# Kernel tuning notes

Hardware: AMD Instinct MI355X
Metric: run time of the kernel (lower is better)

The kernel has to match this reference:

```python
import jax, jax.numpy as jnp
import numpy as np

N = 10000          # num nodes
E = 640000         # num edges (avg degree 64)
IN_CH = 128
OUT_CH = 128


def setup_inputs() -> dict:
    key = jax.random.key(0)
    k_x, k_ei, k_ea, k_w1, k_b1, k_w2, k_b2 = jax.random.split(key, 7)
    x = jax.random.normal(k_x, (N, IN_CH), dtype=jnp.float32)
    edge_index = jax.random.randint(k_ei, (2, E), 0, N, dtype=jnp.int64)
    edge_attr = jax.random.uniform(k_ea, (E,), dtype=jnp.float32)
    # MLP params: Linear(2*in, out) -> ReLU -> Linear(out, out), stored as [in, out]
    s1 = 1.0 / np.sqrt(2 * IN_CH)
    s2 = 1.0 / np.sqrt(OUT_CH)
    W1 = jax.random.uniform(k_w1, (2 * IN_CH, OUT_CH), jnp.float32, -s1, s1)
    b1 = jax.random.uniform(k_b1, (OUT_CH,), jnp.float32, -s1, s1)
    W2 = jax.random.uniform(k_w2, (OUT_CH, OUT_CH), jnp.float32, -s2, s2)
    b2 = jax.random.uniform(k_b2, (OUT_CH,), jnp.float32, -s2, s2)
    return {"x": x, "edge_index": edge_index, "edge_attr": edge_attr,
            "W1": W1, "b1": b1, "W2": W2, "b2": b2}


def reference(x, edge_index, edge_attr, W1, b1, W2, b2):
    row, col = edge_index[0], edge_index[1]
    # message: scale sender feature by edge_attr, concat with receiver feature, 2-layer MLP
    x_i = x[row] * edge_attr[:, None]          # [E, in]
    x_j = x[col]                               # [E, in]
    combined = jnp.concatenate([x_i, x_j], axis=1)  # [E, 2*in]
    h = jax.nn.relu(combined @ W1 + b1)        # [E, out]
    messages = h @ W2 + b2                     # [E, out]
    # sum aggregation: scatter-add messages into receiving nodes (col)
    out = jnp.zeros((x.shape[0], messages.shape[1]), dtype=messages.dtype)
    out = out.at[col].add(messages)
    return out
```

## Files before the change

### kernel.cpp

```cpp
#include <hip/hip_runtime.h>

#define C 128
#define NPB 16
#define NSLAB 8
#define CAP8 24
#define OVF_MAX 65536
#define EPT 4

typedef int   vi4 __attribute__((ext_vector_type(4)));
typedef float vf4 __attribute__((ext_vector_type(4)));

__device__ __forceinline__ unsigned bf16_bits(float x) {
    unsigned u = __float_as_uint(x);
    u += 0x7FFFu + ((u >> 16) & 1u);
    return u >> 16;
}
__device__ __forceinline__ float bf16f(unsigned short b) {
    return __uint_as_float(((unsigned)b) << 16);
}
__device__ __forceinline__ int xcd_id() {
    return (int)(__builtin_amdgcn_s_getreg(63508) & 7u);
}

__global__ void fused_pre_kernel(const float* __restrict__ x, const float* __restrict__ W1,
                                 unsigned short* __restrict__ P16, float* __restrict__ Q,
                                 const int* __restrict__ ei, const float* __restrict__ attr,
                                 int* __restrict__ cursor, int* __restrict__ ovf_cnt,
                                 int2* __restrict__ ovf, unsigned* __restrict__ sorted,
                                 int N, int E, int SB) {
    if ((int)blockIdx.x < SB) {
        const int slab = xcd_id();
        int* __restrict__ cur = cursor + (size_t)slab * N;
        unsigned* __restrict__ sl = sorted + ((size_t)slab * N) * CAP8;
        const int base = (blockIdx.x * 256 + threadIdx.x) * EPT;
        if (base >= E) return;
        if (base + EPT <= E) {
            const vi4 r0 = __builtin_nontemporal_load((const vi4*)(ei + base));
            const vi4 c0 = __builtin_nontemporal_load((const vi4*)(ei + (size_t)E + base));
            const vf4 a0 = __builtin_nontemporal_load((const vf4*)(attr + base));
            const int rows[EPT] = {r0.x, r0.y, r0.z, r0.w};
            const int cols[EPT] = {c0.x, c0.y, c0.z, c0.w};
            const float as[EPT] = {a0.x, a0.y, a0.z, a0.w};
            int pos[EPT];
#pragma unroll
            for (int j = 0; j < EPT; ++j)
                pos[j] = atomicAdd(&cur[cols[j]], 1);
#pragma unroll
            for (int j = 0; j < EPT; ++j) {
                const unsigned v = (bf16_bits(as[j]) << 16) | (unsigned)rows[j];
                if (pos[j] < CAP8) {
                    sl[(size_t)cols[j] * CAP8 + pos[j]] = v;
                } else {
                    const int o = atomicAdd(ovf_cnt, 1);
                    if (o < OVF_MAX) ovf[o] = make_int2(cols[j], (int)v);
                }
            }
        } else {
            for (int e = base; e < E; ++e) {
                const int row = ei[e], colv = ei[(size_t)E + e];
                const int pos = atomicAdd(&cur[colv], 1);
                const unsigned v = (bf16_bits(attr[e]) << 16) | (unsigned)row;
                if (pos < CAP8) sl[(size_t)colv * CAP8 + pos] = v;
                else {
                    const int o = atomicAdd(ovf_cnt, 1);
                    if (o < OVF_MAX) ovf[o] = make_int2(colv, (int)v);
                }
            }
        }
    } else {
        __shared__ float xs[NPB][C];
        const int pb = blockIdx.x - SB;
        const int n0 = pb * NPB;
        const int tt = threadIdx.x & (C - 1);
        const int half = threadIdx.x >> 7;
        for (int i = threadIdx.x; i < NPB * C; i += 256) {
            const int gi = n0 * C + i;
            xs[0][i] = (gi < N * C) ? __builtin_nontemporal_load(x + gi) : 0.f;
        }
        __syncthreads();
        const float* __restrict__ Wb = W1 + (half ? (C * C) : 0) + tt;
        float acc[NPB] = {};
        for (int k = 0; k < C; ++k) {
            const float w = Wb[k * C];
#pragma unroll
            for (int j = 0; j < NPB; ++j)
                acc[j] = fmaf(xs[j][k], w, acc[j]);
        }
#pragma unroll
        for (int j = 0; j < NPB; ++j)
            if (n0 + j < N) {
                if (half) Q[(size_t)(n0 + j) * C + tt] = acc[j];
                else      P16[(size_t)(n0 + j) * C + tt] = (unsigned short)bf16_bits(acc[j]);
            }
    }
}

struct G { ushort4 p; float a; };
__device__ __forceinline__ G gat(unsigned v, const unsigned short* __restrict__ P16, int ch4) {
    G g;
    g.p = *(const ushort4*)(P16 + (((size_t)(v & 0xFFFFu)) << 7) + (ch4 << 2));
    g.a = __uint_as_float(v & 0xFFFF0000u);
    return g;
}
__device__ __forceinline__ void upd(float4& acc, const G& g, const float4& qb) {
    acc.x += fmaxf(fmaf(g.a, bf16f(g.p.x), qb.x), 0.f);
    acc.y += fmaxf(fmaf(g.a, bf16f(g.p.y), qb.y), 0.f);
    acc.z += fmaxf(fmaf(g.a, bf16f(g.p.z), qb.z), 0.f);
    acc.w += fmaxf(fmaf(g.a, bf16f(g.p.w), qb.w), 0.f);
}

__global__ void agg_out_kernel(const unsigned* __restrict__ sorted, const int* __restrict__ cursor,
                               const unsigned short* __restrict__ P16, const float* __restrict__ Q,
                               const float* __restrict__ b1, const float* __restrict__ W2,
                               const float* __restrict__ b2,
                               const int* __restrict__ ovf_cnt, const int2* __restrict__ ovf,
                               float* __restrict__ out, int N) {
    __shared__ float4 part[2][4][32];
    __shared__ float hs[2][C];
    const int t = threadIdx.x;
    const int j = t >> 7;
    const int slice = (t >> 5) & 3;
    const int ch4 = t & 31;
    const int n = blockIdx.x * 2 + j;

    float4 acc = make_float4(0.f, 0.f, 0.f, 0.f);
    float4 qb = acc;
    int deg = 0;
    if (n < N) {
        int cnts[NSLAB];
#pragma unroll
        for (int s = 0; s < NSLAB; ++s) {
            cnts[s] = cursor[(size_t)s * N + n];
            deg += cnts[s];
        }
        const float4 q4  = *(const float4*)(Q + (size_t)n * C + (ch4 << 2));
        const float4 b14 = *(const float4*)(b1 + (ch4 << 2));
        qb = make_float4(q4.x + b14.x, q4.y + b14.y, q4.z + b14.z, q4.w + b14.w);
#pragma unroll
        for (int si = 0; si < 2; ++si) {
            const int s = slice + (si << 2);
            const int cs = min(cnts[s], CAP8);
            const unsigned* __restrict__ buf = sorted + ((size_t)s * N + n) * CAP8;
            int i = 0;
            for (; i + 4 <= cs; i += 4) {
                const uint4 v = *(const uint4*)(buf + i);
                const G g0 = gat(v.x, P16, ch4), g1 = gat(v.y, P16, ch4);
                const G g2 = gat(v.z, P16, ch4), g3 = gat(v.w, P16, ch4);
                upd(acc, g0, qb); upd(acc, g1, qb); upd(acc, g2, qb); upd(acc, g3, qb);
            }
            for (; i < cs; ++i) {
                const G g = gat(buf[i], P16, ch4);
                upd(acc, g, qb);
            }
        }
        const int oc = min(*ovf_cnt, OVF_MAX);
        if (oc > 0 && slice == 0) {
            for (int o = 0; o < oc; ++o) {
                const int2 v = ovf[o];
                if (v.x == n) { const G g = gat((unsigned)v.y, P16, ch4); upd(acc, g, qb); }
            }
        }
    }
    part[j][slice][ch4] = acc;
    __syncthreads();
    if (slice == 0 && n < N) {
        const float4 r0 = part[j][0][ch4], r1 = part[j][1][ch4];
        const float4 r2 = part[j][2][ch4], r3 = part[j][3][ch4];
        float4 h;
        h.x = r0.x + r1.x + r2.x + r3.x;
        h.y = r0.y + r1.y + r2.y + r3.y;
        h.z = r0.z + r1.z + r2.z + r3.z;
        h.w = r0.w + r1.w + r2.w + r3.w;
        *(float4*)(&hs[j][ch4 << 2]) = h;
    }
    __syncthreads();
    float4 o = make_float4(0.f, 0.f, 0.f, 0.f);
    if (n < N) {
        const int k0 = slice << 5;
#pragma unroll 8
        for (int k = k0; k < k0 + 32; ++k) {
            const float hv = hs[j][k];
            const float4 w = *(const float4*)(W2 + (size_t)k * C + (ch4 << 2));
            o.x = fmaf(hv, w.x, o.x);
            o.y = fmaf(hv, w.y, o.y);
            o.z = fmaf(hv, w.z, o.z);
            o.w = fmaf(hv, w.w, o.w);
        }
    }
    __syncthreads();
    part[j][slice][ch4] = o;
    __syncthreads();
    if (slice == 0 && n < N) {
        const float4 r0 = part[j][0][ch4], r1 = part[j][1][ch4];
        const float4 r2 = part[j][2][ch4], r3 = part[j][3][ch4];
        const float4 b24 = *(const float4*)(b2 + (ch4 << 2));
        const float d = (float)deg;
        float4 res;
        res.x = fmaf(d, b24.x, r0.x + r1.x + r2.x + r3.x);
        res.y = fmaf(d, b24.y, r0.y + r1.y + r2.y + r3.y);
        res.z = fmaf(d, b24.z, r0.z + r1.z + r2.z + r3.z);
        res.w = fmaf(d, b24.w, r0.w + r1.w + r2.w + r3.w);
        *(float4*)(out + (size_t)n * C + (ch4 << 2)) = res;
    }
}

extern "C" void kernel_launch(void* const* d_in, const int* in_sizes, int n_in,
                              void* d_out, int out_size, void* d_ws, size_t ws_size,
                              hipStream_t stream) {
    const float* x    = (const float*)d_in[0];
    const int*   ei   = (const int*)d_in[1];
    const float* attr = (const float*)d_in[2];
    const float* W1   = (const float*)d_in[3];
    const float* b1   = (const float*)d_in[4];
    const float* W2   = (const float*)d_in[5];
    const float* b2   = (const float*)d_in[6];
    float* out = (float*)d_out;

    const int N = in_sizes[0] / C;
    const int E = in_sizes[2];

    char* ws = (char*)d_ws;
    unsigned short* P16 = (unsigned short*)ws;  ws += (size_t)N * C * sizeof(unsigned short);
    ws = (char*)(((uintptr_t)ws + 15) & ~(uintptr_t)15);
    float*    Q       = (float*)ws;     ws += (size_t)N * C * sizeof(float);
    unsigned* sorted  = (unsigned*)ws;  ws += (size_t)NSLAB * N * CAP8 * sizeof(unsigned);
    int2*     ovf     = (int2*)ws;      ws += (size_t)OVF_MAX * sizeof(int2);
    int*      cursor  = (int*)ws;       ws += (size_t)NSLAB * N * sizeof(int);
    int*      ovf_cnt = (int*)ws;

    (void)hipMemsetAsync(cursor, 0, ((size_t)NSLAB * N + 1) * sizeof(int), stream);

    const int SB = (E + 256 * EPT - 1) / (256 * EPT);
    const int PB = (N + NPB - 1) / NPB;
    fused_pre_kernel<<<SB + PB, 256, 0, stream>>>(x, W1, P16, Q, ei, attr,
                                                  cursor, ovf_cnt, ovf, sorted, N, E, SB);
    agg_out_kernel<<<(N + 1) / 2, 256, 0, stream>>>(sorted, cursor, P16, Q, b1, W2, b2,
                                                    ovf_cnt, ovf, out, N);
}
```

Baseline: 161.3 us.

## Assign one 16-lane group per slab in aggregation and halve edges per thread in bucketing

```diff
diff --git a/kernel.cpp b/kernel.cpp
--- a/kernel.cpp
+++ b/kernel.cpp
@@ -5,18 +5,15 @@
 #define NSLAB 8
 #define CAP8 24
 #define OVF_MAX 65536
-#define EPT 4
-
-typedef int   vi4 __attribute__((ext_vector_type(4)));
-typedef float vf4 __attribute__((ext_vector_type(4)));
+#define EPT 2
+
+typedef int   vi2 __attribute__((ext_vector_type(2)));
+typedef float vf2 __attribute__((ext_vector_type(2)));
 
 __device__ __forceinline__ unsigned bf16_bits(float x) {
     unsigned u = __float_as_uint(x);
     u += 0x7FFFu + ((u >> 16) & 1u);
     return u >> 16;
-}
-__device__ __forceinline__ float bf16f(unsigned short b) {
-    return __uint_as_float(((unsigned)b) << 16);
 }
 __device__ __forceinline__ int xcd_id() {
     return (int)(__builtin_amdgcn_s_getreg(63508) & 7u);
@@ -35,36 +32,24 @@
         const int base = (blockIdx.x * 256 + threadIdx.x) * EPT;
         if (base >= E) return;
         if (base + EPT <= E) {
-            const vi4 r0 = __builtin_nontemporal_load((const vi4*)(ei + base));
-            const vi4 c0 = __builtin_nontemporal_load((const vi4*)(ei + (size_t)E + base));
-            const vf4 a0 = __builtin_nontemporal_load((const vf4*)(attr + base));
-            const int rows[EPT] = {r0.x, r0.y, r0.z, r0.w};
-            const int cols[EPT] = {c0.x, c0.y, c0.z, c0.w};
-            const float as[EPT] = {a0.x, a0.y, a0.z, a0.w};
-            int pos[EPT];
-#pragma unroll
-            for (int j = 0; j < EPT; ++j)
-                pos[j] = atomicAdd(&cur[cols[j]], 1);
-#pragma unroll
-            for (int j = 0; j < EPT; ++j) {
-                const unsigned v = (bf16_bits(as[j]) << 16) | (unsigned)rows[j];
-                if (pos[j] < CAP8) {
-                    sl[(size_t)cols[j] * CAP8 + pos[j]] = v;
-                } else {
-                    const int o = atomicAdd(ovf_cnt, 1);
-                    if (o < OVF_MAX) ovf[o] = make_int2(cols[j], (int)v);
-                }
-            }
+            const vi2 r = __builtin_nontemporal_load((const vi2*)(ei + base));
+            const vi2 c = __builtin_nontemporal_load((const vi2*)(ei + (size_t)E + base));
+            const vf2 a = __builtin_nontemporal_load((const vf2*)(attr + base));
+            const int pos0 = atomicAdd(&cur[c.x], 1);
+            const int pos1 = atomicAdd(&cur[c.y], 1);
+            const unsigned v0 = (bf16_bits(a.x) << 16) | (unsigned)r.x;
+            const unsigned v1 = (bf16_bits(a.y) << 16) | (unsigned)r.y;
+            if (pos0 < CAP8) sl[(size_t)c.x * CAP8 + pos0] = v0;
+            else { const int o = atomicAdd(ovf_cnt, 1); if (o < OVF_MAX) ovf[o] = make_int2(c.x, (int)v0); }
+            if (pos1 < CAP8) sl[(size_t)c.y * CAP8 + pos1] = v1;
+            else { const int o = atomicAdd(ovf_cnt, 1); if (o < OVF_MAX) ovf[o] = make_int2(c.y, (int)v1); }
         } else {
             for (int e = base; e < E; ++e) {
                 const int row = ei[e], colv = ei[(size_t)E + e];
                 const int pos = atomicAdd(&cur[colv], 1);
                 const unsigned v = (bf16_bits(attr[e]) << 16) | (unsigned)row;
                 if (pos < CAP8) sl[(size_t)colv * CAP8 + pos] = v;
-                else {
-                    const int o = atomicAdd(ovf_cnt, 1);
-                    if (o < OVF_MAX) ovf[o] = make_int2(colv, (int)v);
-                }
+                else { const int o = atomicAdd(ovf_cnt, 1); if (o < OVF_MAX) ovf[o] = make_int2(colv, (int)v); }
             }
         }
     } else {
@@ -95,85 +80,87 @@
     }
 }
 
-struct G { ushort4 p; float a; };
-__device__ __forceinline__ G gat(unsigned v, const unsigned short* __restrict__ P16, int ch4) {
-    G g;
-    g.p = *(const ushort4*)(P16 + (((size_t)(v & 0xFFFFu)) << 7) + (ch4 << 2));
-    g.a = __uint_as_float(v & 0xFFFF0000u);
-    return g;
-}
-__device__ __forceinline__ void upd(float4& acc, const G& g, const float4& qb) {
-    acc.x += fmaxf(fmaf(g.a, bf16f(g.p.x), qb.x), 0.f);
-    acc.y += fmaxf(fmaf(g.a, bf16f(g.p.y), qb.y), 0.f);
-    acc.z += fmaxf(fmaf(g.a, bf16f(g.p.z), qb.z), 0.f);
-    acc.w += fmaxf(fmaf(g.a, bf16f(g.p.w), qb.w), 0.f);
-}
-
 __global__ void agg_out_kernel(const unsigned* __restrict__ sorted, const int* __restrict__ cursor,
                                const unsigned short* __restrict__ P16, const float* __restrict__ Q,
                                const float* __restrict__ b1, const float* __restrict__ W2,
                                const float* __restrict__ b2,
                                const int* __restrict__ ovf_cnt, const int2* __restrict__ ovf,
                                float* __restrict__ out, int N) {
-    __shared__ float4 part[2][4][32];
+    __shared__ float part8[2][NSLAB][16][9];
     __shared__ float hs[2][C];
+    __shared__ int   degs[2][NSLAB];
+    __shared__ float4 part4[2][4][32];
     const int t = threadIdx.x;
     const int j = t >> 7;
+    const int s = (t >> 4) & 7;
+    const int l = t & 15;
+    const int n = blockIdx.x * 2 + j;
+
+    float acc[8] = {};
+    if (n < N) {
+        const int rawcnt = cursor[(size_t)s * N + n];
+        if (l == 0) degs[j][s] = rawcnt;
+        const int cnt = min(rawcnt, CAP8);
+        float qb[8];
+        {
+            const float4 qa = *(const float4*)(Q + (size_t)n * C + l * 8);
+            const float4 qc = *(const float4*)(Q + (size_t)n * C + l * 8 + 4);
+            const float4 ba = *(const float4*)(b1 + l * 8);
+            const float4 bb = *(const float4*)(b1 + l * 8 + 4);
+            qb[0] = qa.x + ba.x; qb[1] = qa.y + ba.y; qb[2] = qa.z + ba.z; qb[3] = qa.w + ba.w;
+            qb[4] = qc.x + bb.x; qb[5] = qc.y + bb.y; qb[6] = qc.z + bb.z; qb[7] = qc.w + bb.w;
+        }
+        const unsigned* __restrict__ buf = sorted + ((size_t)s * N + n) * CAP8;
+        for (int i = 0; i < cnt; ++i) {
+            const unsigned v = buf[i];
+            const uint4 pw = *(const uint4*)(P16 + (((size_t)(v & 0xFFFFu)) << 7) + l * 8);
+            const float a = __uint_as_float(v & 0xFFFF0000u);
+            const float p0 = __uint_as_float(pw.x << 16), p1 = __uint_as_float(pw.x & 0xFFFF0000u);
+            const float p2 = __uint_as_float(pw.y << 16), p3 = __uint_as_float(pw.y & 0xFFFF0000u);
+            const float p4 = __uint_as_float(pw.z << 16), p5 = __uint_as_float(pw.z & 0xFFFF0000u);
+            const float p6 = __uint_as_float(pw.w << 16), p7 = __uint_as_float(pw.w & 0xFFFF0000u);
+            acc[0] += fmaxf(fmaf(a, p0, qb[0]), 0.f);
+            acc[1] += fmaxf(fmaf(a, p1, qb[1]), 0.f);
+            acc[2] += fmaxf(fmaf(a, p2, qb[2]), 0.f);
+            acc[3] += fmaxf(fmaf(a, p3, qb[3]), 0.f);
+            acc[4] += fmaxf(fmaf(a, p4, qb[4]), 0.f);
+            acc[5] += fmaxf(fmaf(a, p5, qb[5]), 0.f);
+            acc[6] += fmaxf(fmaf(a, p6, qb[6]), 0.f);
+            acc[7] += fmaxf(fmaf(a, p7, qb[7]), 0.f);
+        }
+        const int oc = min(*ovf_cnt, OVF_MAX);
+        if (oc > 0 && s == 0) {
+            for (int o = 0; o < oc; ++o) {
+                const int2 v = ovf[o];
+                if (v.x == n) {
+                    const unsigned u = (unsigned)v.y;
+                    const uint4 pw = *(const uint4*)(P16 + (((size_t)(u & 0xFFFFu)) << 7) + l * 8);
+                    const float a = __uint_as_float(u & 0xFFFF0000u);
+                    acc[0] += fmaxf(fmaf(a, __uint_as_float(pw.x << 16), qb[0]), 0.f);
+                    acc[1] += fmaxf(fmaf(a, __uint_as_float(pw.x & 0xFFFF0000u), qb[1]), 0.f);
+                    acc[2] += fmaxf(fmaf(a, __uint_as_float(pw.y << 16), qb[2]), 0.f);
+                    acc[3] += fmaxf(fmaf(a, __uint_as_float(pw.y & 0xFFFF0000u), qb[3]), 0.f);
+                    acc[4] += fmaxf(fmaf(a, __uint_as_float(pw.z << 16), qb[4]), 0.f);
+                    acc[5] += fmaxf(fmaf(a, __uint_as_float(pw.z & 0xFFFF0000u), qb[5]), 0.f);
+                    acc[6] += fmaxf(fmaf(a, __uint_as_float(pw.w << 16), qb[6]), 0.f);
+                    acc[7] += fmaxf(fmaf(a, __uint_as_float(pw.w & 0xFFFF0000u), qb[7]), 0.f);
+                }
+            }
+        }
+    }
+#pragma unroll
+    for (int k = 0; k < 8; ++k) part8[j][s][l][k] = acc[k];
+    __syncthreads();
+    {
+        const int ch = t & 127;
+        float h = 0.f;
+#pragma unroll
+        for (int ss = 0; ss < NSLAB; ++ss) h += part8[j][ss][ch >> 3][ch & 7];
+        hs[j][ch] = h;
+    }
+    __syncthreads();
     const int slice = (t >> 5) & 3;
     const int ch4 = t & 31;
-    const int n = blockIdx.x * 2 + j;
-
-    float4 acc = make_float4(0.f, 0.f, 0.f, 0.f);
-    float4 qb = acc;
-    int deg = 0;
-    if (n < N) {
-        int cnts[NSLAB];
-#pragma unroll
-        for (int s = 0; s < NSLAB; ++s) {
-            cnts[s] = cursor[(size_t)s * N + n];
-            deg += cnts[s];
-        }
-        const float4 q4  = *(const float4*)(Q + (size_t)n * C + (ch4 << 2));
-        const float4 b14 = *(const float4*)(b1 + (ch4 << 2));
-        qb = make_float4(q4.x + b14.x, q4.y + b14.y, q4.z + b14.z, q4.w + b14.w);
-#pragma unroll
-        for (int si = 0; si < 2; ++si) {
-            const int s = slice + (si << 2);
-            const int cs = min(cnts[s], CAP8);
-            const unsigned* __restrict__ buf = sorted + ((size_t)s * N + n) * CAP8;
-            int i = 0;
-            for (; i + 4 <= cs; i += 4) {
-                const uint4 v = *(const uint4*)(buf + i);
-                const G g0 = gat(v.x, P16, ch4), g1 = gat(v.y, P16, ch4);
-                const G g2 = gat(v.z, P16, ch4), g3 = gat(v.w, P16, ch4);
-                upd(acc, g0, qb); upd(acc, g1, qb); upd(acc, g2, qb); upd(acc, g3, qb);
-            }
-            for (; i < cs; ++i) {
-                const G g = gat(buf[i], P16, ch4);
-                upd(acc, g, qb);
-            }
-        }
-        const int oc = min(*ovf_cnt, OVF_MAX);
-        if (oc > 0 && slice == 0) {
-            for (int o = 0; o < oc; ++o) {
-                const int2 v = ovf[o];
-                if (v.x == n) { const G g = gat((unsigned)v.y, P16, ch4); upd(acc, g, qb); }
-            }
-        }
-    }
-    part[j][slice][ch4] = acc;
-    __syncthreads();
-    if (slice == 0 && n < N) {
-        const float4 r0 = part[j][0][ch4], r1 = part[j][1][ch4];
-        const float4 r2 = part[j][2][ch4], r3 = part[j][3][ch4];
-        float4 h;
-        h.x = r0.x + r1.x + r2.x + r3.x;
-        h.y = r0.y + r1.y + r2.y + r3.y;
-        h.z = r0.z + r1.z + r2.z + r3.z;
-        h.w = r0.w + r1.w + r2.w + r3.w;
-        *(float4*)(&hs[j][ch4 << 2]) = h;
-    }
-    __syncthreads();
     float4 o = make_float4(0.f, 0.f, 0.f, 0.f);
     if (n < N) {
         const int k0 = slice << 5;
@@ -187,12 +174,14 @@
             o.w = fmaf(hv, w.w, o.w);
         }
     }
-    __syncthreads();
-    part[j][slice][ch4] = o;
+    part4[j][slice][ch4] = o;
     __syncthreads();
     if (slice == 0 && n < N) {
-        const float4 r0 = part[j][0][ch4], r1 = part[j][1][ch4];
-        const float4 r2 = part[j][2][ch4], r3 = part[j][3][ch4];
+        const float4 r0 = part4[j][0][ch4], r1 = part4[j][1][ch4];
+        const float4 r2 = part4[j][2][ch4], r3 = part4[j][3][ch4];
+        int deg = 0;
+#pragma unroll
+        for (int ss = 0; ss < NSLAB; ++ss) deg += degs[j][ss];
         const float4 b24 = *(const float4*)(b2 + (ch4 << 2));
         const float d = (float)deg;
         float4 res;
```

New measurement: 171.7 us. 6.4% more time.
